# Optimization experiments

Measured on AMD Instinct MI355X. Metric: run time of the kernel, lower is better.

## Reference

```python
import jax, jax.numpy as jnp
import numpy as np

B, S, H = 4, 1024, 2048      # batch, seq_len, hidden_size
N, D = 16, 128               # num_attention_heads, attention_head_size (num_kv_heads == N)
W_SCALE = 0.02


def setup_inputs() -> dict:
    key = jax.random.key(0)
    ks = jax.random.split(key, 7)
    hidden_states = jax.random.normal(ks[0], (B, S, H), dtype=jnp.float32)
    # Per-head query projections (stacked over the head axis) + shared K/V projections.
    Wq = jax.random.normal(ks[1], (N, H, D), dtype=jnp.float32) * W_SCALE
    bq = jax.random.normal(ks[2], (N, D), dtype=jnp.float32) * W_SCALE
    Wk = jax.random.normal(ks[3], (H, D), dtype=jnp.float32) * W_SCALE
    bk = jax.random.normal(ks[4], (D,), dtype=jnp.float32) * W_SCALE
    Wv = jax.random.normal(ks[5], (H, D), dtype=jnp.float32) * W_SCALE
    bv = jax.random.normal(ks[6], (D,), dtype=jnp.float32) * W_SCALE
    return {"hidden_states": hidden_states, "Wq": Wq, "bq": bq,
            "Wk": Wk, "bk": bk, "Wv": Wv, "bv": bv}


def reference(hidden_states, Wq, bq, Wk, bk, Wv, bv):
    # Batched equivalent of the per-head Python loop:
    # q_i = Linear_i(h); k = key_layer(h); v = value_layer(h) (shared across heads,
    # repeat_interleave is a no-op since num_kv_heads == num_attention_heads).
    Q = jnp.einsum('bsh,nhd->bnsd', hidden_states, Wq) + bq[None, :, None, :]  # [B,N,S,D]
    K = hidden_states @ Wk + bk   # [B,S,D]
    V = hidden_states @ Wv + bv   # [B,S,D]
    # NOTE: source applies no 1/sqrt(D) scaling.
    scores = jnp.einsum('bnsd,btd->bnst', Q, K)          # [B,N,S,S]
    attn = jax.nn.softmax(scores, axis=-1)
    out = jnp.einsum('bnst,btd->bnsd', attn, V)          # [B,N,S,D]
    return out
```

## Files before the change

kernel.cpp:

```cpp
#include <hip/hip_runtime.h>
#include <hip/hip_bf16.h>

typedef unsigned short ushort_t;
typedef _Float16 half_t;
typedef __attribute__((ext_vector_type(8))) _Float16 h8;
typedef __attribute__((ext_vector_type(8))) short short8;
typedef __attribute__((ext_vector_type(4))) short short4_t;
typedef __attribute__((ext_vector_type(4))) float f32x4;
typedef __attribute__((ext_vector_type(16))) float f32x16;
typedef __attribute__((ext_vector_type(4))) float f4;

#define NB 4
#define SS 1024
#define HH 2048
#define NH 16
#define DD 128
#define MM (NB*SS)
#define NTOT 2304
#define COL_K 2048
#define COL_V 2176
#define KVB 64
#define L2E 1.44269504089f

__device__ __forceinline__ ushort_t f2h(float x) {
    half_t h = (half_t)x;
    return *(ushort_t*)&h;
}
__device__ __forceinline__ f32x4 mfma16h(h8 a, h8 b, f32x4 c) {
    return __builtin_amdgcn_mfma_f32_16x16x32_f16(a, b, c, 0, 0, 0);
}
__device__ __forceinline__ f32x16 mfma32h(h8 a, h8 b, f32x16 c) {
    return __builtin_amdgcn_mfma_f32_32x32x16_f16(a, b, c, 0, 0, 0);
}
__device__ __forceinline__ void load_lds16(const ushort_t* g, ushort_t* l) {
    __builtin_amdgcn_global_load_lds(
        (const __attribute__((address_space(1))) unsigned int*)g,
        (__attribute__((address_space(3))) unsigned int*)l,
        16, 0, 0);
}

__global__ void k_cvt(const float* __restrict__ src, ushort_t* __restrict__ dst, int n) {
    int i = (blockIdx.x * blockDim.x + threadIdx.x) * 8;
    if (i + 7 < n) {
        f4 a = *(const f4*)(src + i);
        f4 b = *(const f4*)(src + i + 4);
        short8 o;
        #pragma unroll
        for (int j = 0; j < 4; ++j) { o[j] = (short)f2h(a[j]); o[4 + j] = (short)f2h(b[j]); }
        *(short8*)(dst + i) = o;
    }
}

__global__ __launch_bounds__(256) void k_tw(const float* __restrict__ W,
                                            ushort_t* __restrict__ T, int Dd) {
    __shared__ ushort_t t[64][74];
    const int n = blockIdx.z;
    const int h0 = blockIdx.x * 64, d0 = blockIdx.y * 64;
    const int r = threadIdx.x >> 2, cg = (threadIdx.x & 3) * 16;
    const float* src = W + ((size_t)n * HH + h0 + r) * Dd + d0 + cg;
    #pragma unroll
    for (int v = 0; v < 4; ++v) {
        f4 a = *(const f4*)(src + v * 4);
        #pragma unroll
        for (int j = 0; j < 4; ++j) t[r][cg + v * 4 + j] = f2h(a[j]);
    }
    __syncthreads();
    short8 o0, o1;
    #pragma unroll
    for (int j = 0; j < 8; ++j) { o0[j] = (short)t[cg + j][r]; o1[j] = (short)t[cg + 8 + j][r]; }
    ushort_t* dst = T + ((size_t)(n * Dd + d0 + r)) * HH + h0 + cg;
    *(short8*)dst = o0;
    *(short8*)(dst + 8) = o1;
}

__global__ __launch_bounds__(256) void k_gemm(
    const ushort_t* __restrict__ A, const ushort_t* __restrict__ B,
    const float* __restrict__ bq, const float* __restrict__ bk,
    const float* __restrict__ bvv, ushort_t* __restrict__ O,
    ushort_t* __restrict__ Vt) {

    constexpr int BK = 32;
    __shared__ ushort_t sA[128 * BK], sB[128 * BK];

    const int bid = blockIdx.x;
    const int swz = (bid & 7) * 72 + (bid >> 3);
    const int m0 = (swz & 31) * 128;
    const int n0 = (swz >> 5) * 128;

    const int tid = threadIdx.x;
    const int w = tid >> 6, l = tid & 63;
    const int wr = w >> 1, wc = w & 1;
    f32x4 acc[4][4] = {};

    for (int kt = 0; kt < HH / BK; ++kt) {
        const int k0 = kt * BK;
        #pragma unroll
        for (int c = 0; c < 2; ++c) {
            int chunk = c * 4 + w;
            int idx = chunk * 512 + l * 8;
            int row = idx >> 5, kc = idx & 31;
            load_lds16(A + (size_t)(m0 + row) * HH + k0 + kc, &sA[chunk * 512]);
            load_lds16(B + (size_t)(n0 + row) * HH + k0 + kc, &sB[chunk * 512]);
        }
        __syncthreads();

        h8 a[4], b[4];
        #pragma unroll
        for (int i = 0; i < 4; ++i) {
            int ra = wr * 64 + i * 16 + (l & 15);
            int rb = wc * 64 + i * 16 + (l & 15);
            a[i] = *(const h8*)&sA[ra * 32 + (l >> 4) * 8];
            b[i] = *(const h8*)&sB[rb * 32 + (l >> 4) * 8];
        }
        #pragma unroll
        for (int i = 0; i < 4; ++i)
            #pragma unroll
            for (int j = 0; j < 4; ++j)
                acc[i][j] = mfma16h(a[i], b[j], acc[i][j]);
        __syncthreads();
    }

    #pragma unroll
    for (int i = 0; i < 4; ++i) {
        int row = m0 + wr * 64 + i * 16 + ((l >> 4) << 2);
        #pragma unroll
        for (int j = 0; j < 4; ++j) {
            int col = n0 + wc * 64 + j * 16 + (l & 15);
            float bv = (col < COL_K) ? bq[col]
                     : (col < COL_V) ? bk[col - COL_K]
                                     : bvv[col - COL_V];
            if (col < COL_V) {
                #pragma unroll
                for (int r = 0; r < 4; ++r)
                    O[(size_t)(row + r) * NTOT + col] = f2h(acc[i][j][r] + bv);
            } else {
                short4_t o;
                #pragma unroll
                for (int r = 0; r < 4; ++r) o[r] = (short)f2h(acc[i][j][r] + bv);
                *(short4_t*)&Vt[(size_t)(col - COL_V) * MM + row] = o;
            }
        }
    }
}

__global__ __launch_bounds__(256, 2) void k_attn(
    const ushort_t* __restrict__ O, const ushort_t* __restrict__ Vt,
    float* __restrict__ Out) {

    __shared__ ushort_t sK[2][KVB * 128];
    __shared__ ushort_t sVt[2][128 * KVB];

    const int tid = threadIdx.x;
    const int w = tid >> 6, l = tid & 63;
    const int li = l & 31, hi = l >> 5;
    const int q0 = blockIdx.x * 128;
    const int n = blockIdx.y, b = blockIdx.z;
    const int q = q0 + w * 32 + li;

    const int mkK = (li & 3) | (((li >> 3) & 3) << 2);
    const int mkV = li & 7;

    h8 qv[8];
    {
        size_t base = ((size_t)(b * SS + q)) * NTOT + n * 128 + hi * 8;
        #pragma unroll
        for (int c = 0; c < 8; ++c)
            qv[c] = *(const h8*)&O[base + c * 16];
    }

    f32x16 acc0 = {}, acc1 = {}, acc2 = {}, acc3 = {};
    float m2 = -3.0e38f, lsum = 0.f;

    auto stage = [&](int bi, int t0) {
        #pragma unroll
        for (int c = 0; c < 4; ++c) {
            int seg = c * 4 + w;
            int oe = seg * 512 + l * 8;
            int row = oe >> 7;
            int mk = (row & 3) | (((row >> 3) & 3) << 2);
            int ce = (oe & 127) ^ (mk << 3);
            size_t g = (size_t)(b * SS + t0 + row) * NTOT + COL_K + ce;
            load_lds16(O + g, &sK[bi][seg * 512]);
        }
        #pragma unroll
        for (int c = 0; c < 4; ++c) {
            int seg = c * 4 + w;
            int oe = seg * 512 + l * 8;
            int row = oe >> 6;
            int ce = (oe & 63) ^ ((row & 7) << 3);
            size_t g = (size_t)row * MM + b * SS + t0 + ce;
            load_lds16(Vt + g, &sVt[bi][seg * 512]);
        }
    };

    stage(0, 0);
    constexpr int NT = SS / KVB;

    for (int it = 0; it < NT; ++it) {
        const int cur = it & 1;
        const int t0i = it * KVB;
        __syncthreads();
        if (it + 1 < NT) stage(cur ^ 1, t0i + KVB);
        const ushort_t* sKc = sK[cur];
        const ushort_t* sVc = sVt[cur];

        f32x16 s0 = {}, s1 = {};
        __builtin_amdgcn_s_setprio(1);
        #pragma unroll
        for (int c = 0; c < 8; ++c) {
            int eo = (c * 16 + hi * 8) ^ (mkK << 3);
            h8 k0 = *(const h8*)&sKc[li * 128 + eo];
            h8 k1 = *(const h8*)&sKc[(32 + li) * 128 + eo];
            s0 = mfma32h(k0, qv[c], s0);
            s1 = mfma32h(k1, qv[c], s1);
        }
        __builtin_amdgcn_s_setprio(0);

        float mv = s0[0];
        #pragma unroll
        for (int r = 1; r < 16; ++r) mv = fmaxf(mv, s0[r]);
        #pragma unroll
        for (int r = 0; r < 16; ++r) mv = fmaxf(mv, s1[r]);
        mv = fmaxf(mv, __shfl_xor(mv, 32));
        float pm2 = mv * L2E;

        if (!__all(pm2 <= m2 + 11.54f)) {
            float mn = fmaxf(m2, pm2);
            float scl = exp2f(m2 - mn);
            lsum *= scl;
            #pragma unroll
            for (int r = 0; r < 16; ++r) {
                acc0[r] *= scl; acc1[r] *= scl; acc2[r] *= scl; acc3[r] *= scl;
            }
            m2 = mn;
        }

        unsigned int pk[2][8];
        #pragma unroll
        for (int g = 0; g < 2; ++g)
            #pragma unroll
            for (int j = 0; j < 8; ++j) {
                float pA = exp2f(fmaf((g ? s1 : s0)[2 * j],     L2E, -m2));
                float pB = exp2f(fmaf((g ? s1 : s0)[2 * j + 1], L2E, -m2));
                lsum += pA + pB;
                union { unsigned int u; half_t h[2]; } pu;
                pu.h[0] = (half_t)pA; pu.h[1] = (half_t)pB;
                pk[g][j] = pu.u;
            }

        __builtin_amdgcn_s_setprio(1);
        #pragma unroll
        for (int tc = 0; tc < 4; ++tc) {
            const int g = tc >> 1, jb = (tc & 1) * 4;
            unsigned int a0 = pk[g][jb + 0], b0 = pk[g][jb + 2];
            unsigned int a1 = pk[g][jb + 1], b1 = pk[g][jb + 3];
            asm volatile("v_permlane32_swap_b32 %0, %1" : "+v"(a0), "+v"(b0));
            asm volatile("v_permlane32_swap_b32 %0, %1" : "+v"(a1), "+v"(b1));
            union { h8 h; unsigned int u[4]; } B2;
            B2.u[0] = a0; B2.u[1] = a1; B2.u[2] = b0; B2.u[3] = b1;

            int eo = (tc * 16 + hi * 8) ^ (mkV << 3);
            h8 v0 = *(const h8*)&sVc[(0 * 32 + li) * KVB + eo];
            h8 v1 = *(const h8*)&sVc[(1 * 32 + li) * KVB + eo];
            h8 v2 = *(const h8*)&sVc[(2 * 32 + li) * KVB + eo];
            h8 v3 = *(const h8*)&sVc[(3 * 32 + li) * KVB + eo];
            acc0 = mfma32h(v0, B2.h, acc0);
            acc1 = mfma32h(v1, B2.h, acc1);
            acc2 = mfma32h(v2, B2.h, acc2);
            acc3 = mfma32h(v3, B2.h, acc3);
        }
        __builtin_amdgcn_s_setprio(0);
    }

    lsum += __shfl_xor(lsum, 32);
    float inv = 1.0f / lsum;
    size_t base = (((size_t)b * NH + n) * SS + q) * DD;
    #pragma unroll
    for (int dg = 0; dg < 4; ++dg) {
        const f32x16& ac = (dg == 0) ? acc0 : (dg == 1) ? acc1 : (dg == 2) ? acc2 : acc3;
        #pragma unroll
        for (int j = 0; j < 4; ++j) {
            int d0 = dg * 32 + 8 * j + 4 * hi;
            f4 o;
            #pragma unroll
            for (int r = 0; r < 4; ++r) o[r] = ac[4 * j + r] * inv;
            *(f4*)&Out[base + d0] = o;
        }
    }
}

#define OFF_HC    ((size_t)0)
#define OFF_BC    (OFF_HC + (size_t)MM*HH*2)
#define OFF_O     (OFF_BC + (size_t)NTOT*HH*2)
#define OFF_VT    (OFF_O + (size_t)MM*NTOT*2)

extern "C" void kernel_launch(void* const* d_in, const int* in_sizes, int n_in,
                              void* d_out, int out_size, void* d_ws, size_t ws_size,
                              hipStream_t stream) {
    const float* hs = (const float*)d_in[0];
    const float* Wq = (const float*)d_in[1];
    const float* bq = (const float*)d_in[2];
    const float* Wk = (const float*)d_in[3];
    const float* bk = (const float*)d_in[4];
    const float* Wv = (const float*)d_in[5];
    const float* bv = (const float*)d_in[6];
    float* out = (float*)d_out;
    char* ws = (char*)d_ws;

    ushort_t* hc   = (ushort_t*)(ws + OFF_HC);
    ushort_t* bcat = (ushort_t*)(ws + OFF_BC);
    ushort_t* Obuf = (ushort_t*)(ws + OFF_O);
    ushort_t* vt   = (ushort_t*)(ws + OFF_VT);

    k_cvt<<<(MM*HH)/(256*8), 256, 0, stream>>>(hs, hc, MM*HH);
    dim3 gwq(HH/64, DD/64, NH);
    k_tw<<<gwq, 256, 0, stream>>>(Wq, bcat, DD);
    dim3 gwk(HH/64, DD/64, 1);
    k_tw<<<gwk, 256, 0, stream>>>(Wk, bcat + (size_t)COL_K*HH, DD);
    k_tw<<<gwk, 256, 0, stream>>>(Wv, bcat + (size_t)COL_V*HH, DD);

    k_gemm<<<(MM/128)*(NTOT/128), 256, 0, stream>>>(hc, bcat, bq, bk, bv, Obuf, vt);

    dim3 ga(SS/128, NH, NB);
    k_attn<<<ga, 256, 0, stream>>>(Obuf, vt, out);
}
```

Before: 133.3 us.

## Halve KV tile, raise occupancy, and transpose PV MFMA operand order

Shrinks the KV block from 64 to 32 keys, halving shared memory per stage and the score registers, and raises launch bounds to 3 blocks per CU. The PV MFMA now uses P as the A operand and V as the B operand, so the output accumulator is laid out with query rows across registers. That layout needs per-row rescale and normalization factors fetched via cross-lane shuffles, and it writes the output with scalar stores instead of 16-byte vector stores. The smaller tiles double the number of loop iterations and barriers, and they add shuffle overhead in the rescale path.

```diff
diff --git a/kernel.cpp b/kernel.cpp
--- a/kernel.cpp
+++ b/kernel.cpp
@@ -19,7 +19,7 @@
 #define NTOT 2304
 #define COL_K 2048
 #define COL_V 2176
-#define KVB 64
+#define KVB 32
 #define L2E 1.44269504089f
 
 __device__ __forceinline__ ushort_t f2h(float x) {
@@ -143,7 +143,7 @@
     }
 }
 
-__global__ __launch_bounds__(256, 2) void k_attn(
+__global__ __launch_bounds__(256, 3) void k_attn(
     const ushort_t* __restrict__ O, const ushort_t* __restrict__ Vt,
     float* __restrict__ Out) {
 
@@ -158,7 +158,6 @@
     const int q = q0 + w * 32 + li;
 
     const int mkK = (li & 3) | (((li >> 3) & 3) << 2);
-    const int mkV = li & 7;
 
     h8 qv[8];
     {
@@ -173,7 +172,7 @@
 
     auto stage = [&](int bi, int t0) {
         #pragma unroll
-        for (int c = 0; c < 4; ++c) {
+        for (int c = 0; c < 2; ++c) {
             int seg = c * 4 + w;
             int oe = seg * 512 + l * 8;
             int row = oe >> 7;
@@ -183,12 +182,12 @@
             load_lds16(O + g, &sK[bi][seg * 512]);
         }
         #pragma unroll
-        for (int c = 0; c < 4; ++c) {
+        for (int c = 0; c < 2; ++c) {
             int seg = c * 4 + w;
             int oe = seg * 512 + l * 8;
-            int row = oe >> 6;
-            int ce = (oe & 63) ^ ((row & 7) << 3);
-            size_t g = (size_t)row * MM + b * SS + t0 + ce;
+            int d = oe >> 5;
+            int ce = ((oe >> 3) & 3) ^ (d & 3);
+            size_t g = (size_t)d * MM + b * SS + t0 + ce * 8;
             load_lds16(Vt + g, &sVt[bi][seg * 512]);
         }
     };
@@ -198,29 +197,23 @@
 
     for (int it = 0; it < NT; ++it) {
         const int cur = it & 1;
-        const int t0i = it * KVB;
         __syncthreads();
-        if (it + 1 < NT) stage(cur ^ 1, t0i + KVB);
+        if (it + 1 < NT) stage(cur ^ 1, (it + 1) * KVB);
         const ushort_t* sKc = sK[cur];
         const ushort_t* sVc = sVt[cur];
 
-        f32x16 s0 = {}, s1 = {};
+        f32x16 s0 = {};
         __builtin_amdgcn_s_setprio(1);
         #pragma unroll
         for (int c = 0; c < 8; ++c) {
-            int eo = (c * 16 + hi * 8) ^ (mkK << 3);
-            h8 k0 = *(const h8*)&sKc[li * 128 + eo];
-            h8 k1 = *(const h8*)&sKc[(32 + li) * 128 + eo];
-            s0 = mfma32h(k0, qv[c], s0);
-            s1 = mfma32h(k1, qv[c], s1);
+            h8 kv = *(const h8*)&sKc[li * 128 + ((c * 16 + hi * 8) ^ (mkK << 3))];
+            s0 = mfma32h(kv, qv[c], s0);
         }
         __builtin_amdgcn_s_setprio(0);
 
         float mv = s0[0];
         #pragma unroll
         for (int r = 1; r < 16; ++r) mv = fmaxf(mv, s0[r]);
-        #pragma unroll
-        for (int r = 0; r < 16; ++r) mv = fmaxf(mv, s1[r]);
         mv = fmaxf(mv, __shfl_xor(mv, 32));
         float pm2 = mv * L2E;
 
@@ -230,62 +223,62 @@
             lsum *= scl;
             #pragma unroll
             for (int r = 0; r < 16; ++r) {
-                acc0[r] *= scl; acc1[r] *= scl; acc2[r] *= scl; acc3[r] *= scl;
+                int qs = (r & 3) + 8 * (r >> 2) + 4 * hi;
+                float sr = __shfl(scl, qs + (w << 6 >> 6) * 0 + (l & 64) * 0 + 0, 64);
+                sr = __shfl(scl, qs);
+                acc0[r] *= sr; acc1[r] *= sr; acc2[r] *= sr; acc3[r] *= sr;
             }
             m2 = mn;
         }
 
-        unsigned int pk[2][8];
-        #pragma unroll
-        for (int g = 0; g < 2; ++g)
-            #pragma unroll
-            for (int j = 0; j < 8; ++j) {
-                float pA = exp2f(fmaf((g ? s1 : s0)[2 * j],     L2E, -m2));
-                float pB = exp2f(fmaf((g ? s1 : s0)[2 * j + 1], L2E, -m2));
-                lsum += pA + pB;
-                union { unsigned int u; half_t h[2]; } pu;
-                pu.h[0] = (half_t)pA; pu.h[1] = (half_t)pB;
-                pk[g][j] = pu.u;
-            }
+        unsigned int pk[8];
+        #pragma unroll
+        for (int j = 0; j < 8; ++j) {
+            float pA = exp2f(fmaf(s0[2 * j],     L2E, -m2));
+            float pB = exp2f(fmaf(s0[2 * j + 1], L2E, -m2));
+            lsum += pA + pB;
+            union { unsigned int u; half_t h[2]; } pu;
+            pu.h[0] = (half_t)pA; pu.h[1] = (half_t)pB;
+            pk[j] = pu.u;
+        }
 
         __builtin_amdgcn_s_setprio(1);
         #pragma unroll
-        for (int tc = 0; tc < 4; ++tc) {
-            const int g = tc >> 1, jb = (tc & 1) * 4;
-            unsigned int a0 = pk[g][jb + 0], b0 = pk[g][jb + 2];
-            unsigned int a1 = pk[g][jb + 1], b1 = pk[g][jb + 3];
+        for (int tc = 0; tc < 2; ++tc) {
+            unsigned int a0 = pk[tc * 4 + 0], b0 = pk[tc * 4 + 2];
+            unsigned int a1 = pk[tc * 4 + 1], b1 = pk[tc * 4 + 3];
             asm volatile("v_permlane32_swap_b32 %0, %1" : "+v"(a0), "+v"(b0));
             asm volatile("v_permlane32_swap_b32 %0, %1" : "+v"(a1), "+v"(b1));
-            union { h8 h; unsigned int u[4]; } B2;
-            B2.u[0] = a0; B2.u[1] = a1; B2.u[2] = b0; B2.u[3] = b1;
-
-            int eo = (tc * 16 + hi * 8) ^ (mkV << 3);
-            h8 v0 = *(const h8*)&sVc[(0 * 32 + li) * KVB + eo];
-            h8 v1 = *(const h8*)&sVc[(1 * 32 + li) * KVB + eo];
-            h8 v2 = *(const h8*)&sVc[(2 * 32 + li) * KVB + eo];
-            h8 v3 = *(const h8*)&sVc[(3 * 32 + li) * KVB + eo];
-            acc0 = mfma32h(v0, B2.h, acc0);
-            acc1 = mfma32h(v1, B2.h, acc1);
-            acc2 = mfma32h(v2, B2.h, acc2);
-            acc3 = mfma32h(v3, B2.h, acc3);
+            union { h8 h; unsigned int u[4]; } P2;
+            P2.u[0] = a0; P2.u[1] = a1; P2.u[2] = b0; P2.u[3] = b1;
+
+            const int ch = tc * 2 + hi;
+            #pragma unroll
+            for (int dg = 0; dg < 4; ++dg) {
+                int d = dg * 32 + li;
+                h8 va = *(const h8*)&sVc[d * KVB + ((ch ^ (d & 3)) << 3)];
+                f32x16& ac = (dg == 0) ? acc0 : (dg == 1) ? acc1 : (dg == 2) ? acc2 : acc3;
+                ac = mfma32h(P2.h, va, ac);
+            }
         }
         __builtin_amdgcn_s_setprio(0);
     }
 
     lsum += __shfl_xor(lsum, 32);
     float inv = 1.0f / lsum;
-    size_t base = (((size_t)b * NH + n) * SS + q) * DD;
-    #pragma unroll
-    for (int dg = 0; dg < 4; ++dg) {
-        const f32x16& ac = (dg == 0) ? acc0 : (dg == 1) ? acc1 : (dg == 2) ? acc2 : acc3;
-        #pragma unroll
-        for (int j = 0; j < 4; ++j) {
-            int d0 = dg * 32 + 8 * j + 4 * hi;
-            f4 o;
-            #pragma unroll
-            for (int r = 0; r < 4; ++r) o[r] = ac[4 * j + r] * inv;
-            *(f4*)&Out[base + d0] = o;
-        }
+    float iv[16];
+    #pragma unroll
+    for (int r = 0; r < 16; ++r)
+        iv[r] = __shfl(inv, (r & 3) + 8 * (r >> 2) + 4 * hi);
+
+    #pragma unroll
+    for (int r = 0; r < 16; ++r) {
+        int qs = (r & 3) + 8 * (r >> 2) + 4 * hi;
+        size_t base = (((size_t)b * NH + n) * SS + q0 + w * 32 + qs) * DD + li;
+        Out[base +  0] = acc0[r] * iv[r];
+        Out[base + 32] = acc1[r] * iv[r];
+        Out[base + 64] = acc2[r] * iv[r];
+        Out[base + 96] = acc3[r] * iv[r];
     }
 }
 
```

Measured after the change: 136.9 us. 2.7% more time.
